# Kernel tuning notes

Measured on AMD Instinct MI355X. Metric: run time of the kernel, lower is better.

The kernel has to match this reference:

```python
import jax, jax.numpy as jnp
import numpy as np
from jax import lax

N = 120000      # total real voxels
C = 128         # d_model
NH = 8          # heads
HD = C // NH    # head dim
T = 36          # window capacity
FILL = 24       # real tokens per window
NW = N // FILL  # 5000 windows
L = 4           # encoder layers (num_blocks=2, 2 layers each)
DFF = 256
B, H, Wd = 2, 320, 320
SCALE = HD ** -0.5


def setup_inputs() -> dict:
    key = jax.random.key(0)
    ks = jax.random.split(key, 16)
    voxel_feats = jax.random.normal(ks[0], (N, C), jnp.float32)
    # shift-0 window assignment: contiguous; shift-1: random permutation of voxels
    base = jnp.arange(N, dtype=jnp.int32)
    ind0 = (base // FILL) * T + (base % FILL)
    perm = jax.random.permutation(ks[1], N).astype(jnp.int32)
    ind1 = (perm // FILL) * T + (perm % FILL)
    mask = jnp.tile(jnp.arange(T) >= FILL, (NW, 1))  # True = padded key slot
    pos0 = 0.02 * jax.random.normal(ks[2], (NW, T, C), jnp.float32)
    pos1 = 0.02 * jax.random.normal(ks[3], (NW, T, C), jnp.float32)
    bcol = (jnp.arange(N) >= N // 2).astype(jnp.int32)
    yy = jax.random.randint(ks[4], (N,), 0, H, jnp.int32)
    xx = jax.random.randint(ks[5], (N,), 0, Wd, jnp.int32)
    voxel_coors = jnp.stack([bcol, jnp.zeros(N, jnp.int32), yy, xx], axis=1)
    s = 0.02
    return dict(
        voxel_feats=voxel_feats,
        pos0=pos0, pos1=pos1,
        in_proj_w=s * jax.random.normal(ks[6], (L, 3 * C, C), jnp.float32),
        in_proj_b=jnp.zeros((L, 3 * C), jnp.float32),
        out_proj_w=s * jax.random.normal(ks[7], (L, C, C), jnp.float32),
        out_proj_b=jnp.zeros((L, C), jnp.float32),
        lin1_w=s * jax.random.normal(ks[8], (L, DFF, C), jnp.float32),
        lin1_b=jnp.zeros((L, DFF), jnp.float32),
        lin2_w=s * jax.random.normal(ks[9], (L, C, DFF), jnp.float32),
        lin2_b=jnp.zeros((L, C), jnp.float32),
        ln1_w=jnp.ones((L, C), jnp.float32), ln1_b=jnp.zeros((L, C), jnp.float32),
        ln2_w=jnp.ones((L, C), jnp.float32), ln2_b=jnp.zeros((L, C), jnp.float32),
        conv_w=0.05 * jax.random.normal(ks[10], (2, C, C, 3, 3), jnp.float32),
        voxel_coors=voxel_coors, ind0=ind0, ind1=ind1, mask0=mask, mask1=mask,
    )


def _ln(x, w, b):
    m = jnp.mean(x, -1, keepdims=True)
    v = jnp.mean((x - m) ** 2, -1, keepdims=True)
    return (x - m) * lax.rsqrt(v + 1e-5) * w + b


def _encoder_layer(x, ind, pos, mask, ipw, ipb, opw, opb, l1w, l1b, l2w, l2b,
                   n1w, n1b, n2w, n2b):
    # flat2window_v2: scatter flat tokens into padded window buffer
    feat3d = jnp.zeros((NW * T, C), x.dtype).at[ind].set(x).reshape(NW, T, C)
    qk_in = feat3d + pos  # pos added to q and k only
    wq, wk, wv = ipw[:C], ipw[C:2 * C], ipw[2 * C:]
    bq, bk, bv = ipb[:C], ipb[C:2 * C], ipb[2 * C:]
    q = (qk_in @ wq.T + bq).reshape(NW, T, NH, HD)
    k = (qk_in @ wk.T + bk).reshape(NW, T, NH, HD)
    v = (feat3d @ wv.T + bv).reshape(NW, T, NH, HD)
    scores = jnp.einsum('wqhd,wkhd->whqk', q, k) * SCALE
    scores = jnp.where(mask[:, None, None, :], -1e9, scores)  # key padding mask
    attn = jax.nn.softmax(scores, axis=-1)
    o = jnp.einsum('whqk,wkhd->wqhd', attn, v).reshape(NW, T, C)
    o = o @ opw.T + opb
    a = o.reshape(NW * T, C)[ind]  # window2flat_v2: gather valid slots
    x = _ln(x + a, n1w, n1b)       # post_norm residual 1
    f = jax.nn.gelu(x @ l1w.T + l1b, approximate=False) @ l2w.T + l2b
    return _ln(x + f, n2w, n2b)    # post_norm residual 2


def reference(voxel_feats, pos0, pos1, in_proj_w, in_proj_b, out_proj_w,
              out_proj_b, lin1_w, lin1_b, lin2_w, lin2_b, ln1_w, ln1_b,
              ln2_w, ln2_b, conv_w, voxel_coors, ind0, ind1, mask0, mask1):
    x = voxel_feats
    for l in range(L):
        ind, pos, mask = (ind0, pos0, mask0) if l % 2 == 0 else (ind1, pos1, mask1)
        x = _encoder_layer(x, ind, pos, mask, in_proj_w[l], in_proj_b[l],
                           out_proj_w[l], out_proj_b[l], lin1_w[l], lin1_b[l],
                           lin2_w[l], lin2_b[l], ln1_w[l], ln1_b[l],
                           ln2_w[l], ln2_b[l])
    # recover_bev: scatter tokens into dense [B, C, H, W] canvas
    flat = voxel_coors[:, 2] * Wd + voxel_coors[:, 3]
    canvas = jnp.zeros((B, H * Wd, C), x.dtype).at[voxel_coors[:, 0], flat].set(x)
    out = canvas.reshape(B, H, Wd, C).transpose(0, 3, 1, 2)
    for i in range(2):  # attached 3x3 conv (bias=False) + ReLU
        out = jax.nn.relu(lax.conv_general_dilated(
            out, conv_w[i], (1, 1), [(1, 1), (1, 1)],
            dimension_numbers=('NCHW', 'OIHW', 'NCHW')))
    return out
```

## Files before the change

kernel.cpp:

```cpp
#include <hip/hip_runtime.h>
#include <math.h>

#define NVOX 120000
#define CDIM 128
#define NWIN 5000
#define HWPIX 102400

typedef __attribute__((ext_vector_type(8))) short short8;
typedef __attribute__((ext_vector_type(4))) float f32x4;

__device__ __forceinline__ unsigned short f2bf(float f) {
  unsigned u = __float_as_uint(f);
  return (unsigned short)((u + 0x7FFFu + ((u >> 16) & 1u)) >> 16);
}
__device__ __forceinline__ unsigned pack2(float a, float b) {
  return (unsigned)f2bf(a) | ((unsigned)f2bf(b) << 16);
}
__device__ __forceinline__ void unpack2(unsigned u, float& a, float& b) {
  a = __uint_as_float(u << 16);
  b = __uint_as_float(u & 0xFFFF0000u);
}

__device__ __forceinline__ void mma128(const short* __restrict__ As,
                                       const short* __restrict__ Ws,
                                       int aoff, int boff, f32x4 acc[2][4]) {
#pragma unroll
  for (int kc = 0; kc < 4; ++kc) {
    short8 a0 = *(const short8*)(As + aoff + kc * 32);
    short8 a1 = *(const short8*)(As + aoff + 136 * 16 + kc * 32);
#pragma unroll
    for (int nt = 0; nt < 4; ++nt) {
      short8 b = *(const short8*)(Ws + boff + nt * 136 * 16 + kc * 32);
      acc[0][nt] = __builtin_amdgcn_mfma_f32_16x16x32_bf16(a0, b, acc[0][nt], 0, 0, 0);
      acc[1][nt] = __builtin_amdgcn_mfma_f32_16x16x32_bf16(a1, b, acc[1][nt], 0, 0, 0);
    }
  }
}

__global__ __launch_bounds__(256) void cvt_kernel(const float* __restrict__ src,
                                                  unsigned short* __restrict__ dst, int n4) {
  int i = blockIdx.x * 256 + threadIdx.x;
  if (i >= n4) return;
  float4 v = ((const float4*)src)[i];
  uint2 o; o.x = pack2(v.x, v.y); o.y = pack2(v.z, v.w);
  ((uint2*)dst)[i] = o;
}

__global__ __launch_bounds__(256) void cvtT_kernel(const float* __restrict__ w,
                                                   unsigned short* __restrict__ wT) {
  int idx = blockIdx.x * 256 + threadIdx.x;
  if (idx >= 2 * 9 * 128 * 128) return;
  int ci = idx & 127;
  int co = (idx >> 7) & 127;
  int tap = (idx >> 14) % 9;
  int conv = idx / (9 * 16384);
  wT[idx] = f2bf(w[((size_t)(conv * 128 + co) * 128 + ci) * 9 + tap]);
}

__global__ __launch_bounds__(256) void qkv_kernel(
    const unsigned short* __restrict__ x, const float* __restrict__ pos,
    const int* __restrict__ ind, const unsigned short* __restrict__ ipwB,
    const float* __restrict__ ipb, unsigned short* __restrict__ qb,
    unsigned short* __restrict__ kb, unsigned short* __restrict__ vb) {
  __shared__ __align__(16) char ldsraw[52224];
  short* As = (short*)ldsraw;
  short* Ws = (short*)(ldsraw + 17408);
  const int t = threadIdx.x;
  const int lane = t & 63, wv = t >> 6;
  const int l15 = lane & 15, quad = lane >> 4;
  const int rbase = 32 * (wv >> 1), cbase = 64 * (wv & 1);
  const int mbase = blockIdx.x * 64;
  const int sec = blockIdx.y;
  f32x4 acc[2][4];
#pragma unroll
  for (int m = 0; m < 2; ++m)
#pragma unroll
    for (int n = 0; n < 4; ++n) acc[m][n] = (f32x4){0.f, 0.f, 0.f, 0.f};

  for (int fi = t; fi < 1024; fi += 256) {
    int row = fi >> 4, c8 = fi & 15;
    int vox = mbase + row;
    uint4 xv = ((const uint4*)x)[(size_t)vox * 16 + c8];
    if (sec < 2) {
      int s = ind[vox];
      const float4* pp = (const float4*)(pos + (size_t)s * 128 + c8 * 8);
      float4 p0 = pp[0], p1 = pp[1];
      float f0, f1, f2, f3, f4, f5, f6, f7;
      unpack2(xv.x, f0, f1); unpack2(xv.y, f2, f3);
      unpack2(xv.z, f4, f5); unpack2(xv.w, f6, f7);
      xv.x = pack2(f0 + p0.x, f1 + p0.y); xv.y = pack2(f2 + p0.z, f3 + p0.w);
      xv.z = pack2(f4 + p1.x, f5 + p1.y); xv.w = pack2(f6 + p1.z, f7 + p1.w);
    }
    *(uint4*)&As[row * 136 + c8 * 8] = xv;
  }
  for (int fi = t; fi < 2048; fi += 256) {
    int row = fi >> 4, c8 = fi & 15;
    ((uint4*)&Ws[row * 136])[c8] =
        ((const uint4*)(ipwB + (size_t)(sec * 128 + row) * 128))[c8];
  }
  __syncthreads();
  mma128(As, Ws, (rbase + l15) * 136 + quad * 8, (cbase + l15) * 136 + quad * 8, acc);
  __syncthreads();

  short* Ybf = (short*)ldsraw;
#pragma unroll
  for (int nt = 0; nt < 4; ++nt) {
    int col = cbase + nt * 16 + l15;
    float bias = ipb[sec * 128 + col];
#pragma unroll
    for (int mt = 0; mt < 2; ++mt)
#pragma unroll
      for (int r = 0; r < 4; ++r)
        Ybf[(rbase + mt * 16 + quad * 4 + r) * 136 + col] =
            (short)f2bf(acc[mt][nt][r] + bias);
  }
  __syncthreads();
  unsigned short* dst = (sec == 0) ? qb : ((sec == 1) ? kb : vb);
  for (int fi = t; fi < 1024; fi += 256) {
    int row = fi >> 4, c8 = fi & 15;
    int s = ind[mbase + row];
    int slot = (s / 36) * 24 + (s % 36);
    ((uint4*)dst)[(size_t)slot * 16 + c8] = ((const uint4*)&Ybf[row * 136])[c8];
  }
}

__global__ __launch_bounds__(256) void attn_kernel(
    unsigned short* __restrict__ qb, const unsigned short* __restrict__ kb,
    const unsigned short* __restrict__ vb) {
  __shared__ float lds[14112];
  float* Qs = lds;
  float* Ks = lds + 3168;
  float* Vs = lds + 6336;
  float* S = lds + 9504;
  const int t = threadIdx.x;
  const size_t base = (size_t)blockIdx.x * 3072;
  for (int fi = t; fi < 1152; fi += 256) {
    int arr = fi / 384, rem = fi % 384;
    int row = rem >> 4, c8 = rem & 15;
    const unsigned short* src = arr == 0 ? qb : (arr == 1 ? kb : vb);
    uint4 raw = ((const uint4*)(src + base))[row * 16 + c8];
    float* dl = lds + arr * 3168 + row * 132 + c8 * 8;
    unpack2(raw.x, dl[0], dl[1]); unpack2(raw.y, dl[2], dl[3]);
    unpack2(raw.z, dl[4], dl[5]); unpack2(raw.w, dl[6], dl[7]);
  }
  __syncthreads();
  for (int idx = t; idx < 4608; idx += 256) {
    int hh = idx / 576, rem = idx % 576;
    int qq = rem / 24, kk = rem % 24;
    const float* qp = &Qs[qq * 132 + hh * 16];
    const float* kp = &Ks[kk * 132 + hh * 16];
    float s = 0.f;
#pragma unroll
    for (int d = 0; d < 16; ++d) s = fmaf(qp[d], kp[d], s);
    S[idx] = s * 0.25f;
  }
  __syncthreads();
  if (t < 192) {
    float* rowp = &S[t * 24];
    float m = rowp[0];
#pragma unroll
    for (int k2 = 1; k2 < 24; ++k2) m = fmaxf(m, rowp[k2]);
    float sum = 0.f;
#pragma unroll
    for (int k2 = 0; k2 < 24; ++k2) { float e = __expf(rowp[k2] - m); rowp[k2] = e; sum += e; }
    float inv = 1.f / sum;
#pragma unroll
    for (int k2 = 0; k2 < 24; ++k2) rowp[k2] *= inv;
  }
  __syncthreads();
  for (int idx = t; idx < 3072; idx += 256) {
    int hh = idx / 384, rem = idx % 384;
    int qq = rem >> 4, dd = rem & 15;
    const float* pp = &S[hh * 576 + qq * 24];
    const float* vp = &Vs[hh * 16 + dd];
    float o = 0.f;
#pragma unroll
    for (int k2 = 0; k2 < 24; ++k2) o = fmaf(pp[k2], vp[k2 * 132], o);
    qb[base + qq * 128 + hh * 16 + dd] = f2bf(o);
  }
}

__global__ __launch_bounds__(256) void outln_kernel(
    const unsigned short* __restrict__ o, const int* __restrict__ ind,
    const unsigned short* __restrict__ opwB, const float* __restrict__ opb,
    const unsigned short* __restrict__ xres, const float* __restrict__ lnw,
    const float* __restrict__ lnb, unsigned short* __restrict__ hout) {
  __shared__ __align__(16) char ldsraw[52224];
  short* As = (short*)ldsraw;
  short* Ws = (short*)(ldsraw + 17408);
  const int t = threadIdx.x;
  const int lane = t & 63, wv = t >> 6;
  const int l15 = lane & 15, quad = lane >> 4;
  const int rbase = 32 * (wv >> 1), cbase = 64 * (wv & 1);
  const int mbase = blockIdx.x * 64;
  f32x4 acc[2][4];
#pragma unroll
  for (int m = 0; m < 2; ++m)
#pragma unroll
    for (int n = 0; n < 4; ++n) acc[m][n] = (f32x4){0.f, 0.f, 0.f, 0.f};

  for (int fi = t; fi < 1024; fi += 256) {
    int row = fi >> 4, c8 = fi & 15;
    int s = ind[mbase + row];
    int slot = (s / 36) * 24 + (s % 36);
    *(uint4*)&As[row * 136 + c8 * 8] = ((const uint4*)o)[(size_t)slot * 16 + c8];
  }
  for (int fi = t; fi < 2048; fi += 256) {
    int row = fi >> 4, c8 = fi & 15;
    ((uint4*)&Ws[row * 136])[c8] = ((const uint4*)(opwB + (size_t)row * 128))[c8];
  }
  __syncthreads();
  mma128(As, Ws, (rbase + l15) * 136 + quad * 8, (cbase + l15) * 136 + quad * 8, acc);
  __syncthreads();

  float* Yf = (float*)ldsraw;
  float* p1 = (float*)(ldsraw + 33792);
  float* p2 = (float*)(ldsraw + 34816);
  float* Ms = (float*)(ldsraw + 35840);
  float* Rs = (float*)(ldsraw + 36096);
#pragma unroll
  for (int nt = 0; nt < 4; ++nt) {
    int col = cbase + nt * 16 + l15;
    float bias = opb[col];
#pragma unroll
    for (int mt = 0; mt < 2; ++mt)
#pragma unroll
      for (int r = 0; r < 4; ++r)
        Yf[(rbase + mt * 16 + quad * 4 + r) * 132 + col] = acc[mt][nt][r] + bias;
  }
  __syncthreads();
  for (int fi = t; fi < 1024; fi += 256) {
    int row = fi >> 4, c8 = fi & 15;
    uint4 xv = ((const uint4*)xres)[(size_t)(mbase + row) * 16 + c8];
    float* yp = &Yf[row * 132 + c8 * 8];
    float a, b;
    unpack2(xv.x, a, b); yp[0] += a; yp[1] += b;
    unpack2(xv.y, a, b); yp[2] += a; yp[3] += b;
    unpack2(xv.z, a, b); yp[4] += a; yp[5] += b;
    unpack2(xv.w, a, b); yp[6] += a; yp[7] += b;
  }
  __syncthreads();
  {
    int r = t & 63, g = t >> 6;
    float s = 0.f, s2 = 0.f;
    for (int c = g * 32; c < g * 32 + 32; ++c) { float v = Yf[r * 132 + c]; s += v; s2 += v * v; }
    p1[g * 64 + r] = s; p2[g * 64 + r] = s2;
  }
  __syncthreads();
  if (t < 64) {
    float s = p1[t] + p1[64 + t] + p1[128 + t] + p1[192 + t];
    float s2 = p2[t] + p2[64 + t] + p2[128 + t] + p2[192 + t];
    float m = s * (1.f / 128.f);
    float var = s2 * (1.f / 128.f) - m * m;
    Ms[t] = m; Rs[t] = rsqrtf(var + 1e-5f);
  }
  __syncthreads();
  for (int fi = t; fi < 1024; fi += 256) {
    int row = fi >> 4, c8 = fi & 15;
    float m = Ms[row], rr = Rs[row];
    const float* yp = &Yf[row * 132 + c8 * 8];
    uint4 ov;
    float v0, v1;
#define LNPAIR(J, FLD) \
    v0 = (yp[2*J] - m) * rr * lnw[c8*8+2*J] + lnb[c8*8+2*J]; \
    v1 = (yp[2*J+1] - m) * rr * lnw[c8*8+2*J+1] + lnb[c8*8+2*J+1]; \
    ov.FLD = pack2(v0, v1);
    LNPAIR(0, x) LNPAIR(1, y) LNPAIR(2, z) LNPAIR(3, w)
#undef LNPAIR
    ((uint4*)hout)[(size_t)(mbase + row) * 16 + c8] = ov;
  }
}

__global__ __launch_bounds__(256) void ffn1_kernel(
    const unsigned short* __restrict__ h, const unsigned short* __restrict__ w1B,
    const float* __restrict__ b1, unsigned short* __restrict__ ff) {
  __shared__ __align__(16) char ldsraw[52224];
  short* As = (short*)ldsraw;
  short* Ws = (short*)(ldsraw + 17408);
  const int t = threadIdx.x;
  const int lane = t & 63, wv = t >> 6;
  const int l15 = lane & 15, quad = lane >> 4;
  const int rbase = 32 * (wv >> 1), cbase = 64 * (wv & 1);
  const int mbase = blockIdx.x * 64;
  const int by = blockIdx.y;
  f32x4 acc[2][4];
#pragma unroll
  for (int m = 0; m < 2; ++m)
#pragma unroll
    for (int n = 0; n < 4; ++n) acc[m][n] = (f32x4){0.f, 0.f, 0.f, 0.f};

  for (int fi = t; fi < 1024; fi += 256) {
    int row = fi >> 4, c8 = fi & 15;
    *(uint4*)&As[row * 136 + c8 * 8] = ((const uint4*)h)[(size_t)(mbase + row) * 16 + c8];
  }
  for (int fi = t; fi < 2048; fi += 256) {
    int row = fi >> 4, c8 = fi & 15;
    ((uint4*)&Ws[row * 136])[c8] =
        ((const uint4*)(w1B + (size_t)(by * 128 + row) * 128))[c8];
  }
  __syncthreads();
  mma128(As, Ws, (rbase + l15) * 136 + quad * 8, (cbase + l15) * 136 + quad * 8, acc);
  __syncthreads();

  short* Ybf = (short*)ldsraw;
#pragma unroll
  for (int nt = 0; nt < 4; ++nt) {
    int col = cbase + nt * 16 + l15;
    float bias = b1[by * 128 + col];
#pragma unroll
    for (int mt = 0; mt < 2; ++mt)
#pragma unroll
      for (int r = 0; r < 4; ++r) {
        float v = acc[mt][nt][r] + bias;
        float g = 0.5f * v * (1.f + erff(v * 0.70710678f));
        Ybf[(rbase + mt * 16 + quad * 4 + r) * 136 + col] = (short)f2bf(g);
      }
  }
  __syncthreads();
  for (int fi = t; fi < 1024; fi += 256) {
    int row = fi >> 4, c8 = fi & 15;
    ((uint4*)ff)[(size_t)(mbase + row) * 32 + by * 16 + c8] =
        ((const uint4*)&Ybf[row * 136])[c8];
  }
}

__global__ __launch_bounds__(256) void ffn2_kernel(
    const unsigned short* __restrict__ ff, const unsigned short* __restrict__ w2B,
    const float* __restrict__ b2, const unsigned short* __restrict__ hres,
    const float* __restrict__ lnw, const float* __restrict__ lnb,
    unsigned short* __restrict__ xout) {
  __shared__ __align__(16) char ldsraw[52224];
  short* As = (short*)ldsraw;
  short* Ws = (short*)(ldsraw + 17408);
  const int t = threadIdx.x;
  const int lane = t & 63, wv = t >> 6;
  const int l15 = lane & 15, quad = lane >> 4;
  const int rbase = 32 * (wv >> 1), cbase = 64 * (wv & 1);
  const int mbase = blockIdx.x * 64;
  f32x4 acc[2][4];
#pragma unroll
  for (int m = 0; m < 2; ++m)
#pragma unroll
    for (int n = 0; n < 4; ++n) acc[m][n] = (f32x4){0.f, 0.f, 0.f, 0.f};

  for (int k2 = 0; k2 < 2; ++k2) {
    if (k2) __syncthreads();
    for (int fi = t; fi < 1024; fi += 256) {
      int row = fi >> 4, c8 = fi & 15;
      *(uint4*)&As[row * 136 + c8 * 8] =
          ((const uint4*)ff)[(size_t)(mbase + row) * 32 + k2 * 16 + c8];
    }
    for (int fi = t; fi < 2048; fi += 256) {
      int row = fi >> 4, c8 = fi & 15;
      ((uint4*)&Ws[row * 136])[c8] =
          ((const uint4*)(w2B + (size_t)row * 256 + k2 * 128))[c8];
    }
    __syncthreads();
    mma128(As, Ws, (rbase + l15) * 136 + quad * 8, (cbase + l15) * 136 + quad * 8, acc);
  }
  __syncthreads();

  float* Yf = (float*)ldsraw;
  float* p1 = (float*)(ldsraw + 33792);
  float* p2 = (float*)(ldsraw + 34816);
  float* Ms = (float*)(ldsraw + 35840);
  float* Rs = (float*)(ldsraw + 36096);
#pragma unroll
  for (int nt = 0; nt < 4; ++nt) {
    int col = cbase + nt * 16 + l15;
    float bias = b2[col];
#pragma unroll
    for (int mt = 0; mt < 2; ++mt)
#pragma unroll
      for (int r = 0; r < 4; ++r)
        Yf[(rbase + mt * 16 + quad * 4 + r) * 132 + col] = acc[mt][nt][r] + bias;
  }
  __syncthreads();
  for (int fi = t; fi < 1024; fi += 256) {
    int row = fi >> 4, c8 = fi & 15;
    uint4 xv = ((const uint4*)hres)[(size_t)(mbase + row) * 16 + c8];
    float* yp = &Yf[row * 132 + c8 * 8];
    float a, b;
    unpack2(xv.x, a, b); yp[0] += a; yp[1] += b;
    unpack2(xv.y, a, b); yp[2] += a; yp[3] += b;
    unpack2(xv.z, a, b); yp[4] += a; yp[5] += b;
    unpack2(xv.w, a, b); yp[6] += a; yp[7] += b;
  }
  __syncthreads();
  {
    int r = t & 63, g = t >> 6;
    float s = 0.f, s2 = 0.f;
    for (int c = g * 32; c < g * 32 + 32; ++c) { float v = Yf[r * 132 + c]; s += v; s2 += v * v; }
    p1[g * 64 + r] = s; p2[g * 64 + r] = s2;
  }
  __syncthreads();
  if (t < 64) {
    float s = p1[t] + p1[64 + t] + p1[128 + t] + p1[192 + t];
    float s2 = p2[t] + p2[64 + t] + p2[128 + t] + p2[192 + t];
    float m = s * (1.f / 128.f);
    float var = s2 * (1.f / 128.f) - m * m;
    Ms[t] = m; Rs[t] = rsqrtf(var + 1e-5f);
  }
  __syncthreads();
  for (int fi = t; fi < 1024; fi += 256) {
    int row = fi >> 4, c8 = fi & 15;
    float m = Ms[row], rr = Rs[row];
    const float* yp = &Yf[row * 132 + c8 * 8];
    uint4 ov;
    float v0, v1;
#define LNPAIR(J, FLD) \
    v0 = (yp[2*J] - m) * rr * lnw[c8*8+2*J] + lnb[c8*8+2*J]; \
    v1 = (yp[2*J+1] - m) * rr * lnw[c8*8+2*J+1] + lnb[c8*8+2*J+1]; \
    ov.FLD = pack2(v0, v1);
    LNPAIR(0, x) LNPAIR(1, y) LNPAIR(2, z) LNPAIR(3, w)
#undef LNPAIR
    ((uint4*)xout)[(size_t)(mbase + row) * 16 + c8] = ov;
  }
}

__global__ void idx_init_kernel(int* __restrict__ idxmap) {
  int i = blockIdx.x * 256 + threadIdx.x;
  if (i < 2 * HWPIX) idxmap[i] = -1;
}

__global__ void scatter_kernel(const int* __restrict__ coors, int* __restrict__ idxmap) {
  int i = blockIdx.x * 256 + threadIdx.x;
  if (i >= NVOX) return;
  int b = coors[i * 4 + 0], y = coors[i * 4 + 2], xx = coors[i * 4 + 3];
  atomicMax(&idxmap[b * HWPIX + y * 320 + xx], i);
}

__global__ void canvas_kernel(const unsigned short* __restrict__ x,
                              const int* __restrict__ idxmap,
                              unsigned short* __restrict__ canvas) {
  int idx = blockIdx.x * 256 + threadIdx.x;
  if (idx >= 2 * HWPIX * 16) return;
  int cell = idx >> 4, c8 = idx & 15;
  int vox = idxmap[cell];
  uint4 v = {0u, 0u, 0u, 0u};
  if (vox >= 0) v = ((const uint4*)x)[(size_t)vox * 16 + c8];
  ((uint4*)canvas)[idx] = v;
}

template <int NCHW_OUT>
__global__ __launch_bounds__(256) void conv_kernel(
    const unsigned short* __restrict__ in, const unsigned short* __restrict__ wTb,
    void* __restrict__ outp) {
  __shared__ __align__(16) char ldsraw[52768];
  short* patch = (short*)ldsraw;
  short* Wt = (short*)(ldsraw + 17952);
  const int t = threadIdx.x;
  const int lane = t & 63, wv = t >> 6;
  const int l15 = lane & 15, quad = lane >> 4;
  const int rbase = 32 * (wv >> 1), cbase = 64 * (wv & 1);
  const int x0 = blockIdx.x * 64;
  const int y = blockIdx.y;
  const int b = blockIdx.z;
  const unsigned short* inb = in + (size_t)b * HWPIX * 128;
  f32x4 acc[2][4];
#pragma unroll
  for (int m = 0; m < 2; ++m)
#pragma unroll
    for (int n = 0; n < 4; ++n) acc[m][n] = (f32x4){0.f, 0.f, 0.f, 0.f};

  for (int dy = 0; dy < 3; ++dy) {
    __syncthreads();
    int gy = y + dy - 1;
    for (int fi = t; fi < 1056; fi += 256) {
      int col = fi >> 4, c8 = fi & 15;
      int gx = x0 + col - 1;
      uint4 v = {0u, 0u, 0u, 0u};
      if (gy >= 0 && gy < 320 && gx >= 0 && gx < 320)
        v = ((const uint4*)inb)[(size_t)(gy * 320 + gx) * 16 + c8];
      *(uint4*)&patch[col * 136 + c8 * 8] = v;
    }
    for (int dx = 0; dx < 3; ++dx) {
      __syncthreads();
      int tap = dy * 3 + dx;
      for (int fi = t; fi < 2048; fi += 256) {
        int row = fi >> 4, c8 = fi & 15;
        ((uint4*)&Wt[row * 136])[c8] =
            ((const uint4*)(wTb + (size_t)(tap * 128 + row) * 128))[c8];
      }
      __syncthreads();
      mma128(patch, Wt, (rbase + l15 + dx) * 136 + quad * 8,
             (cbase + l15) * 136 + quad * 8, acc);
    }
  }
  __syncthreads();
  if (NCHW_OUT) {
    float* Yf = (float*)ldsraw;
#pragma unroll
    for (int nt = 0; nt < 4; ++nt) {
      int col = cbase + nt * 16 + l15;
#pragma unroll
      for (int mt = 0; mt < 2; ++mt)
#pragma unroll
        for (int r = 0; r < 4; ++r)
          Yf[col * 68 + rbase + mt * 16 + quad * 4 + r] = fmaxf(acc[mt][nt][r], 0.f);
    }
    __syncthreads();
    float* out = (float*)outp;
    for (int fi = t; fi < 2048; fi += 256) {
      int co = fi >> 4, q4 = fi & 15;
      float4 v = *(float4*)&Yf[co * 68 + q4 * 4];
      *(float4*)&out[(size_t)(b * 128 + co) * HWPIX + y * 320 + x0 + q4 * 4] = v;
    }
  } else {
    short* Ybf = (short*)ldsraw;
#pragma unroll
    for (int nt = 0; nt < 4; ++nt) {
      int col = cbase + nt * 16 + l15;
#pragma unroll
      for (int mt = 0; mt < 2; ++mt)
#pragma unroll
        for (int r = 0; r < 4; ++r)
          Ybf[(rbase + mt * 16 + quad * 4 + r) * 136 + col] =
              (short)f2bf(fmaxf(acc[mt][nt][r], 0.f));
    }
    __syncthreads();
    unsigned short* out = (unsigned short*)outp;
    for (int fi = t; fi < 1024; fi += 256) {
      int row = fi >> 4, c8 = fi & 15;
      ((uint4*)out)[((size_t)b * HWPIX + y * 320 + x0 + row) * 16 + c8] =
          ((const uint4*)&Ybf[row * 136])[c8];
    }
  }
}

extern "C" void kernel_launch(void* const* d_in, const int* in_sizes, int n_in,
                              void* d_out, int out_size, void* d_ws, size_t ws_size,
                              hipStream_t stream) {
  const float* voxel_feats = (const float*)d_in[0];
  const float* pos0 = (const float*)d_in[1];
  const float* pos1 = (const float*)d_in[2];
  const float* ipw = (const float*)d_in[3];
  const float* ipb = (const float*)d_in[4];
  const float* opw = (const float*)d_in[5];
  const float* opb = (const float*)d_in[6];
  const float* l1w = (const float*)d_in[7];
  const float* l1b = (const float*)d_in[8];
  const float* l2w = (const float*)d_in[9];
  const float* l2b = (const float*)d_in[10];
  const float* n1w = (const float*)d_in[11];
  const float* n1b = (const float*)d_in[12];
  const float* n2w = (const float*)d_in[13];
  const float* n2b = (const float*)d_in[14];
  const float* convw = (const float*)d_in[15];
  const int* coors = (const int*)d_in[16];
  const int* ind0 = (const int*)d_in[17];
  const int* ind1 = (const int*)d_in[18];

  unsigned short* ws = (unsigned short*)d_ws;
  const size_t NC = (size_t)NVOX * CDIM;
  unsigned short* bx = ws;
  unsigned short* bq = ws + NC;
  unsigned short* bk = ws + 2 * NC;
  unsigned short* bv = ws + 3 * NC;
  unsigned short* bh = ws + 4 * NC;
  unsigned short* bff = ws + 5 * NC;
  unsigned short* wB = ws + 7 * NC;
  unsigned short* ipwB = wB;
  unsigned short* opwB = wB + 196608;
  unsigned short* l1wB = wB + 262144;
  unsigned short* l2wB = wB + 393216;
  unsigned short* convB = wB + 524288;
  int* idxmap = (int*)(wB + 819200);
  unsigned short* canvas = bq;
  unsigned short* c1out = bv;

  cvt_kernel<<<15000, 256, 0, stream>>>(voxel_feats, bx, 3840000);
  cvt_kernel<<<192, 256, 0, stream>>>(ipw, ipwB, 49152);
  cvt_kernel<<<64, 256, 0, stream>>>(opw, opwB, 16384);
  cvt_kernel<<<128, 256, 0, stream>>>(l1w, l1wB, 32768);
  cvt_kernel<<<128, 256, 0, stream>>>(l2w, l2wB, 32768);
  cvtT_kernel<<<1152, 256, 0, stream>>>(convw, convB);

  for (int l = 0; l < 4; ++l) {
    const int* ind = (l & 1) ? ind1 : ind0;
    const float* pos = (l & 1) ? pos1 : pos0;
    qkv_kernel<<<dim3(1875, 3), 256, 0, stream>>>(
        bx, pos, ind, ipwB + (size_t)l * 49152, ipb + l * 384, bq, bk, bv);
    attn_kernel<<<NWIN, 256, 0, stream>>>(bq, bk, bv);
    outln_kernel<<<1875, 256, 0, stream>>>(
        bq, ind, opwB + (size_t)l * 16384, opb + l * 128, bx,
        n1w + l * 128, n1b + l * 128, bh);
    ffn1_kernel<<<dim3(1875, 2), 256, 0, stream>>>(
        bh, l1wB + (size_t)l * 32768, l1b + l * 256, bff);
    ffn2_kernel<<<1875, 256, 0, stream>>>(
        bff, l2wB + (size_t)l * 32768, l2b + l * 128, bh,
        n2w + l * 128, n2b + l * 128, bx);
  }

  idx_init_kernel<<<800, 256, 0, stream>>>(idxmap);
  scatter_kernel<<<(NVOX + 255) / 256, 256, 0, stream>>>(coors, idxmap);
  canvas_kernel<<<12800, 256, 0, stream>>>(bx, idxmap, canvas);

  conv_kernel<0><<<dim3(5, 320, 2), 256, 0, stream>>>(canvas, convB, (void*)c1out);
  conv_kernel<1><<<dim3(5, 320, 2), 256, 0, stream>>>(c1out, convB + 9 * 16384, d_out);
}
```

Measured before the change: 1.607 ms.

## Use zero-padded canvas and 2-row conv tiles with direct global A-loads

The canvas and intermediate conv buffer now use a zero-padded 322-wide layout, which removes the bounds checks. A border kernel zeroes the halo of the intermediate buffer. The conv kernel now computes two output rows per block with a 4x4 MFMA tile per wave and reads activation fragments straight from global memory instead of staging patches in LDS. Weights are double-buffered in LDS with register prefetch of the next tap, which cuts barriers. This relies on L1/L2 caching of the activation reads and uses more registers and LDS.

```diff
diff --git a/kernel.cpp b/kernel.cpp
--- a/kernel.cpp
+++ b/kernel.cpp
@@ -5,6 +5,8 @@
 #define CDIM 128
 #define NWIN 5000
 #define HWPIX 102400
+#define PW 322
+#define PCELLS 103684
 
 typedef __attribute__((ext_vector_type(8))) short short8;
 typedef __attribute__((ext_vector_type(4))) float f32x4;
@@ -434,96 +436,142 @@
                               const int* __restrict__ idxmap,
                               unsigned short* __restrict__ canvas) {
   int idx = blockIdx.x * 256 + threadIdx.x;
-  if (idx >= 2 * HWPIX * 16) return;
+  if (idx >= 2 * PCELLS * 16) return;
   int cell = idx >> 4, c8 = idx & 15;
-  int vox = idxmap[cell];
+  int b = (cell >= PCELLS) ? 1 : 0;
+  cell -= b * PCELLS;
+  int yy = cell / PW, xx = cell - yy * PW;
   uint4 v = {0u, 0u, 0u, 0u};
-  if (vox >= 0) v = ((const uint4*)x)[(size_t)vox * 16 + c8];
+  if (yy >= 1 && yy <= 320 && xx >= 1 && xx <= 320) {
+    int vox = idxmap[b * HWPIX + (yy - 1) * 320 + (xx - 1)];
+    if (vox >= 0) v = ((const uint4*)x)[(size_t)vox * 16 + c8];
+  }
   ((uint4*)canvas)[idx] = v;
+}
+
+__global__ void border_kernel(unsigned short* __restrict__ buf) {
+  int i = blockIdx.x * 256 + threadIdx.x;
+  if (i >= 2 * 1284 * 16) return;
+  int c8 = i & 15, j = i >> 4;
+  int b = (j >= 1284) ? 1 : 0;
+  j -= b * 1284;
+  int cell;
+  if (j < 322) cell = j;
+  else if (j < 644) cell = 321 * PW + (j - 322);
+  else { int j2 = j - 644; cell = (1 + (j2 >> 1)) * PW + (j2 & 1) * 321; }
+  uint4 z = {0u, 0u, 0u, 0u};
+  ((uint4*)buf)[((size_t)b * PCELLS + cell) * 16 + c8] = z;
 }
 
 template <int NCHW_OUT>
 __global__ __launch_bounds__(256) void conv_kernel(
     const unsigned short* __restrict__ in, const unsigned short* __restrict__ wTb,
     void* __restrict__ outp) {
-  __shared__ __align__(16) char ldsraw[52768];
-  short* patch = (short*)ldsraw;
-  short* Wt = (short*)(ldsraw + 17952);
+  __shared__ __align__(16) char ldsraw[67584];
   const int t = threadIdx.x;
   const int lane = t & 63, wv = t >> 6;
   const int l15 = lane & 15, quad = lane >> 4;
-  const int rbase = 32 * (wv >> 1), cbase = 64 * (wv & 1);
+  const int wr = wv >> 1, wc = wv & 1;
   const int x0 = blockIdx.x * 64;
-  const int y = blockIdx.y;
+  const int y0 = blockIdx.y * 2;
   const int b = blockIdx.z;
-  const unsigned short* inb = in + (size_t)b * HWPIX * 128;
-  f32x4 acc[2][4];
-#pragma unroll
-  for (int m = 0; m < 2; ++m)
+  const unsigned short* inb = in + (size_t)b * PCELLS * 128;
+  const int srow = t >> 4, sc8 = t & 15;
+
+  f32x4 acc[4][4];
+#pragma unroll
+  for (int m = 0; m < 4; ++m)
 #pragma unroll
     for (int n = 0; n < 4; ++n) acc[m][n] = (f32x4){0.f, 0.f, 0.f, 0.f};
 
-  for (int dy = 0; dy < 3; ++dy) {
-    __syncthreads();
-    int gy = y + dy - 1;
-    for (int fi = t; fi < 1056; fi += 256) {
-      int col = fi >> 4, c8 = fi & 15;
-      int gx = x0 + col - 1;
-      uint4 v = {0u, 0u, 0u, 0u};
-      if (gy >= 0 && gy < 320 && gx >= 0 && gx < 320)
-        v = ((const uint4*)inb)[(size_t)(gy * 320 + gx) * 16 + c8];
-      *(uint4*)&patch[col * 136 + c8 * 8] = v;
-    }
-    for (int dx = 0; dx < 3; ++dx) {
+  uint4 wreg[8];
+#pragma unroll
+  for (int i = 0; i < 8; ++i)
+    wreg[i] = ((const uint4*)(wTb + (size_t)(i * 16 + srow) * 128))[sc8];
+  {
+    short* W0 = (short*)ldsraw;
+#pragma unroll
+    for (int i = 0; i < 8; ++i)
+      *(uint4*)&W0[(i * 16 + srow) * 132 + sc8 * 8] = wreg[i];
+  }
+  __syncthreads();
+
+#pragma unroll
+  for (int tap = 0; tap < 9; ++tap) {
+    const int dy = tap / 3, dx = tap % 3;
+    const short* Wcur = (const short*)(ldsraw + (tap & 1) * 33792);
+    if (tap < 8) {
+#pragma unroll
+      for (int i = 0; i < 8; ++i)
+        wreg[i] = ((const uint4*)(wTb + (size_t)((tap + 1) * 128 + i * 16 + srow) * 128))[sc8];
+    }
+    const unsigned short* ap =
+        inb + (size_t)((y0 + wr + dy) * PW + x0 + dx + l15) * 128 + quad * 8;
+    const short* bp = Wcur + (wc * 64 + l15) * 132 + quad * 8;
+#pragma unroll
+    for (int kc = 0; kc < 4; ++kc) {
+      short8 av[4], bvv[4];
+#pragma unroll
+      for (int mt = 0; mt < 4; ++mt)
+        av[mt] = *(const short8*)(ap + mt * 16 * 128 + kc * 32);
+#pragma unroll
+      for (int nt = 0; nt < 4; ++nt)
+        bvv[nt] = *(const short8*)(bp + nt * 16 * 132 + kc * 32);
+#pragma unroll
+      for (int mt = 0; mt < 4; ++mt)
+#pragma unroll
+        for (int nt = 0; nt < 4; ++nt)
+          acc[mt][nt] = __builtin_amdgcn_mfma_f32_16x16x32_bf16(av[mt], bvv[nt], acc[mt][nt], 0, 0, 0);
+    }
+    if (tap < 8) {
+      short* Wnxt = (short*)(ldsraw + ((tap + 1) & 1) * 33792);
+#pragma unroll
+      for (int i = 0; i < 8; ++i)
+        *(uint4*)&Wnxt[(i * 16 + srow) * 132 + sc8 * 8] = wreg[i];
       __syncthreads();
-      int tap = dy * 3 + dx;
-      for (int fi = t; fi < 2048; fi += 256) {
-        int row = fi >> 4, c8 = fi & 15;
-        ((uint4*)&Wt[row * 136])[c8] =
-            ((const uint4*)(wTb + (size_t)(tap * 128 + row) * 128))[c8];
-      }
-      __syncthreads();
-      mma128(patch, Wt, (rbase + l15 + dx) * 136 + quad * 8,
-             (cbase + l15) * 136 + quad * 8, acc);
-    }
-  }
-  __syncthreads();
+    }
+  }
+  __syncthreads();
+
   if (NCHW_OUT) {
     float* Yf = (float*)ldsraw;
 #pragma unroll
     for (int nt = 0; nt < 4; ++nt) {
-      int col = cbase + nt * 16 + l15;
-#pragma unroll
-      for (int mt = 0; mt < 2; ++mt)
+      int co = wc * 64 + nt * 16 + l15;
+#pragma unroll
+      for (int mt = 0; mt < 4; ++mt)
 #pragma unroll
         for (int r = 0; r < 4; ++r)
-          Yf[col * 68 + rbase + mt * 16 + quad * 4 + r] = fmaxf(acc[mt][nt][r], 0.f);
+          Yf[co * 129 + wr * 64 + mt * 16 + quad * 4 + r] = fmaxf(acc[mt][nt][r], 0.f);
     }
     __syncthreads();
     float* out = (float*)outp;
-    for (int fi = t; fi < 2048; fi += 256) {
-      int co = fi >> 4, q4 = fi & 15;
-      float4 v = *(float4*)&Yf[co * 68 + q4 * 4];
-      *(float4*)&out[(size_t)(b * 128 + co) * HWPIX + y * 320 + x0 + q4 * 4] = v;
+    for (int fi = t; fi < 4096; fi += 256) {
+      int co = fi >> 5, q4 = fi & 31;
+      int px = q4 * 4;
+      int yy = y0 + (px >> 6), xx = x0 + (px & 63);
+      *(float4*)&out[(size_t)(b * 128 + co) * HWPIX + yy * 320 + xx] =
+          *(const float4*)&Yf[co * 129 + px];
     }
   } else {
     short* Ybf = (short*)ldsraw;
 #pragma unroll
     for (int nt = 0; nt < 4; ++nt) {
-      int col = cbase + nt * 16 + l15;
-#pragma unroll
-      for (int mt = 0; mt < 2; ++mt)
+      int co = wc * 64 + nt * 16 + l15;
+#pragma unroll
+      for (int mt = 0; mt < 4; ++mt)
 #pragma unroll
         for (int r = 0; r < 4; ++r)
-          Ybf[(rbase + mt * 16 + quad * 4 + r) * 136 + col] =
+          Ybf[(wr * 64 + mt * 16 + quad * 4 + r) * 132 + co] =
               (short)f2bf(fmaxf(acc[mt][nt][r], 0.f));
     }
     __syncthreads();
     unsigned short* out = (unsigned short*)outp;
-    for (int fi = t; fi < 1024; fi += 256) {
+    for (int fi = t; fi < 2048; fi += 256) {
       int row = fi >> 4, c8 = fi & 15;
-      ((uint4*)out)[((size_t)b * HWPIX + y * 320 + x0 + row) * 16 + c8] =
-          ((const uint4*)&Ybf[row * 136])[c8];
+      int yy = y0 + (row >> 6) + 1, xx = x0 + (row & 63) + 1;
+      ((uint4*)out)[((size_t)b * PCELLS + yy * PW + xx) * 16 + c8] =
+          ((const uint4*)&Ybf[row * 132])[c8];
     }
   }
 }
@@ -594,8 +642,9 @@
 
   idx_init_kernel<<<800, 256, 0, stream>>>(idxmap);
   scatter_kernel<<<(NVOX + 255) / 256, 256, 0, stream>>>(coors, idxmap);
-  canvas_kernel<<<12800, 256, 0, stream>>>(bx, idxmap, canvas);
-
-  conv_kernel<0><<<dim3(5, 320, 2), 256, 0, stream>>>(canvas, convB, (void*)c1out);
-  conv_kernel<1><<<dim3(5, 320, 2), 256, 0, stream>>>(c1out, convB + 9 * 16384, d_out);
-}
+  canvas_kernel<<<(2 * PCELLS * 16 + 255) / 256, 256, 0, stream>>>(bx, idxmap, canvas);
+  border_kernel<<<(2 * 1284 * 16 + 255) / 256, 256, 0, stream>>>(c1out);
+
+  conv_kernel<0><<<dim3(5, 160, 2), 256, 0, stream>>>(canvas, convB, (void*)c1out);
+  conv_kernel<1><<<dim3(5, 160, 2), 256, 0, stream>>>(c1out, convB + 9 * 16384, d_out);
+}
```

After: 1.759 ms. +9.4%, slower.
